# Performance work log

Hardware: AMD Instinct MI355X
Metric: run time of the kernel (lower is better)

The kernel has to match this reference:

```python
import jax, jax.numpy as jnp
import numpy as np

V = 17  # number of skeleton joints (hard-coded in the torch module)
NUM_SUBSET = 3

def _dam_mask():
    # Reproduces the Python masking loops: zero block [12:17,12:17] and rows/cols {3,6,7,9,10}
    m = np.ones((V, V), np.float32)
    m[12:17, 12:17] = 0.0
    for j in (3, 6, 7, 9, 10):
        m[j, :] = 0.0
        m[:, j] = 0.0
    return jnp.asarray(m)

def setup_inputs() -> dict:
    key = jax.random.key(0)
    ks = jax.random.split(key, 8)
    N, Cin, Cout, T, G = 64, 64, 64, 256, 8
    return {
        "x": jax.random.normal(ks[0], (N, Cin, T, V), jnp.float32),
        "A_base": jax.random.uniform(ks[1], (NUM_SUBSET, V, V), jnp.float32),  # fixed adjacency buffer
        "DA": 0.01 * jax.random.normal(ks[2], (NUM_SUBSET, G, V, V), jnp.float32),   # DecoupleA param
        "DAM": 0.01 * jax.random.normal(ks[3], (NUM_SUBSET, G, V, V), jnp.float32),  # DecoupleAM param (masked, detached)
        "conv_w": jax.random.normal(ks[4], (NUM_SUBSET * Cout, Cin), jnp.float32) * (2.0 / Cin) ** 0.5,  # 1x1 conv
        "conv_b": jnp.zeros((NUM_SUBSET * Cout,), jnp.float32),
        "se_w": jax.random.normal(ks[5], (3,), jnp.float32) * 0.5,  # conv2_1: Conv1d(1,1,k=3,pad=1,no bias)
        "bn_gamma": jnp.full((Cout,), 1e-6, jnp.float32),  # bn_init(bn, 1e-6)
        "bn_beta": jnp.zeros((Cout,), jnp.float32),
    }

def reference(x, A_base, DA, DAM, conv_w, conv_b, se_w, bn_gamma, bn_beta):
    G = DA.shape[1]
    Cout = bn_gamma.shape[0]
    N, Cin, T, _ = x.shape
    # --- adjacency assembly: A (buffer, broadcast over groups) + DecoupleA + masked DecoupleAM ---
    A = A_base[:, None] + DA + DAM * _dam_mask()              # [3, G, V, V]
    # torch .repeat(1, out//groups, 1, 1) tiles along channel axis; + 0.04 from A_final loop
    A_final = jnp.tile(A, (1, Cout // G, 1, 1)) + 0.04        # [3, Cout, V, V]
    # --- 1x1 conv C_in -> 3*C_out ---
    m = jnp.einsum('nctv,kc->nktv', x, conv_w) + conv_b[None, :, None, None]
    m = m.reshape(N, NUM_SUBSET, Cout, T, V)
    # --- grouped adjacency aggregation (A_final has no batch dependence) ---
    m = jnp.einsum('nkctv,kcvw->nctw', m, A_final)            # [N, Cout, T, V]
    # --- SE-style channel attention: global avg pool -> Conv1d(k=3) over channels -> sigmoid gate ---
    p = m.mean(axis=(2, 3))                                   # [N, Cout]
    pp = jnp.pad(p, ((0, 0), (1, 1)))
    g = se_w[0] * pp[:, :-2] + se_w[1] * pp[:, 1:-1] + se_w[2] * pp[:, 2:]
    q = m + m * jax.nn.sigmoid(g)[:, :, None, None]
    # --- BatchNorm2d (training mode: batch stats over N,T,V) ---
    mu = q.mean(axis=(0, 2, 3), keepdims=True)
    var = q.var(axis=(0, 2, 3), keepdims=True)
    q = bn_gamma[None, :, None, None] * (q - mu) * jax.lax.rsqrt(var + 1e-5) + bn_beta[None, :, None, None]
    # --- residual (down == identity since in_channels == out_channels) and ReLU ---
    return jax.nn.relu(q + x)
```

## Files before the change

### kernel.cpp

```cpp
#include <hip/hip_runtime.h>
#include <math.h>

#define NN 64
#define CIN 64
#define COUT 64
#define TT 256
#define VV 17
#define NSUB 3
#define GG 8

#define WS_MB 0
#define WS_WBF 12288
#define WS_PSUM 18432
#define WS_SSQ 22528
#define WS_ACOEF 0
#define WS_BCOEF 4096
#define M2BF_BYTE_OFF 131072ull
#define M2BF_NEED (M2BF_BYTE_OFF + 2ull * 64 * 64 * 256 * 17)

typedef short bh8 __attribute__((ext_vector_type(8)));
typedef float f32x4 __attribute__((ext_vector_type(4)));
typedef float f32x16 __attribute__((ext_vector_type(16)));
typedef unsigned short u16t;

__device__ __forceinline__ unsigned bf16r(float f) {
    unsigned u = __builtin_bit_cast(unsigned, f);
    return (u + 0x7fffu + ((u >> 16) & 1u)) >> 16;
}
__device__ __forceinline__ float bf2f(unsigned us) {
    return __builtin_bit_cast(float, us << 16);
}

__device__ __forceinline__ float mfull(const float* Ab, const float* DA, const float* DAM,
                                       int s, int g, int v, int w) {
    const unsigned bad = (1u << 3) | (1u << 6) | (1u << 7) | (1u << 9) | (1u << 10);
    float mask = ((v >= 12 && w >= 12) || ((bad >> v) & 1) || ((bad >> w) & 1)) ? 0.f : 1.f;
    int src = ((s * GG + g) * VV + v) * VV + w;
    return Ab[(s * VV + v) * VV + w] + DA[src] + DAM[src] * mask + 0.04f;
}

__global__ void gcn_prep(const float* __restrict__ Ab, const float* __restrict__ DA,
                         const float* __restrict__ DAM, const float* __restrict__ convw,
                         float* __restrict__ ws) {
    int t0 = blockIdx.x * 256 + threadIdx.x;
    int stride = gridDim.x * 256;
    u16t* wbf = (u16t*)(ws + WS_WBF);
    for (int i = t0; i < 192 * 64; i += stride) wbf[i] = (u16t)bf16r(convw[i]);
    u16t* mb = (u16t*)(ws + WS_MB);
    for (int i = t0; i < NSUB * GG * 32 * 32; i += stride) {
        int k = i & 31, w = (i >> 5) & 31, g = (i >> 10) & 7, s = i >> 13;
        u16t val = 0;
        if (w < VV && k < VV) val = (u16t)bf16r(mfull(Ab, DA, DAM, s, g, k, w));
        mb[i] = val;
    }
    for (int i = t0; i < 8192; i += stride) ws[WS_PSUM + i] = 0.f;
}

template <int BFOUT>
__global__ __launch_bounds__(512, 4) void gcn_pass1(const float* __restrict__ x,
                                                    const float* __restrict__ convb,
                                                    const float* __restrict__ ws,
                                                    float* __restrict__ out,
                                                    u16t* __restrict__ m2b,
                                                    float* __restrict__ psum,
                                                    float* __restrict__ ssq) {
    __shared__ __align__(16) unsigned char smem[73984];
    u16t* xsT = (u16t*)smem;
    u16t* Wl = (u16t*)(smem + 20736);
    u16t* mt = (u16t*)(smem + 48384);

    const int tid = threadIdx.x;
    const int wv = tid >> 6;
    const int l = tid & 63;
    const int c16 = l & 15;
    const int q4 = (l >> 4) & 3;
    const int c32 = l & 31;
    const int hi = l >> 5;
    const int n = blockIdx.x >> 3;

    {
        const unsigned* wsrc = (const unsigned*)(ws + WS_WBF);
        unsigned* wd = (unsigned*)Wl;
        for (int j = tid; j < 192 * 32; j += 512) wd[(j >> 5) * 36 + (j & 31)] = wsrc[j];
        unsigned* mz = (unsigned*)mt;
        for (int j = tid; j < 6400; j += 512) mz[j] = 0u;
    }

    const u16t* mb16 = (const u16t*)(ws + WS_MB);
    bh8 Badj[3], Badj2[3];
#pragma unroll
    for (int s = 0; s < 3; ++s) {
        const u16t* mrow = &mb16[((s * 8 + wv) * 32 + c32) * 32 + 8 * hi];
        Badj[s] = *(const bh8*)mrow;
        Badj2[s] = *(const bh8*)(mrow + 16);
    }

    float acc1[8], acc2[8];
#pragma unroll
    for (int j = 0; j < 8; ++j) { acc1[j] = 0.f; acc2[j] = 0.f; }

    for (int k4 = 0; k4 < 4; ++k4) {
        const int tt = (blockIdx.x & 7) * 4 + k4;

        const float* xb = x + (size_t)n * 64 * 4352 + tt * 136;
        for (int task = tid; task < 136 * 8; task += 512) {
            int oct = task / 136;
            int col = task - 136 * oct;
            const float* src = xb + (8 * oct) * 4352 + col;
            float r0 = src[0], r1 = src[4352], r2 = src[2 * 4352], r3 = src[3 * 4352];
            float r4 = src[4 * 4352], r5 = src[5 * 4352], r6 = src[6 * 4352], r7 = src[7 * 4352];
            uint4 pk;
            pk.x = bf16r(r0) | (bf16r(r1) << 16);
            pk.y = bf16r(r2) | (bf16r(r3) << 16);
            pk.z = bf16r(r4) | (bf16r(r5) << 16);
            pk.w = bf16r(r6) | (bf16r(r7) << 16);
            *(uint4*)&((unsigned*)xsT)[col * 36 + oct * 4] = pk;
        }
        __syncthreads();

        bh8 Bc[2], Bc8[2];
#pragma unroll
        for (int ks = 0; ks < 2; ++ks)
            Bc[ks] = *(const bh8*)&xsT[(16 * wv + c16) * 72 + 32 * ks + 8 * q4];
        if (wv < 4) {
#pragma unroll
            for (int ks = 0; ks < 2; ++ks)
                Bc8[ks] = *(const bh8*)&xsT[(128 + c16) * 72 + 32 * ks + 8 * q4];
        }

        f32x16 D2[2];
        D2[0] = 0; D2[1] = 0;

#pragma unroll
        for (int s = 0; s < 3; ++s) {
            f32x4 Dc[4], Dc8;
#pragma unroll
            for (int rf = 0; rf < 4; ++rf)
                Dc[rf] = *(const f32x4*)(convb + s * 64 + 16 * rf + 4 * q4);
            if (wv < 4) Dc8 = *(const f32x4*)(convb + s * 64 + 16 * wv + 4 * q4);
#pragma unroll
            for (int ks = 0; ks < 2; ++ks)
#pragma unroll
                for (int rf = 0; rf < 4; ++rf) {
                    bh8 A = *(const bh8*)&Wl[(s * 64 + 16 * rf + c16) * 72 + 32 * ks + 8 * q4];
                    Dc[rf] = __builtin_amdgcn_mfma_f32_16x16x32_bf16(A, Bc[ks], Dc[rf], 0, 0, 0);
                }
            if (wv < 4) {
#pragma unroll
                for (int ks = 0; ks < 2; ++ks) {
                    bh8 A = *(const bh8*)&Wl[(s * 64 + 16 * wv + c16) * 72 + 32 * ks + 8 * q4];
                    Dc8 = __builtin_amdgcn_mfma_f32_16x16x32_bf16(A, Bc8[ks], Dc8, 0, 0, 0);
                }
            }

            if (s > 0) __syncthreads();
            {
                int col = 16 * wv + c16;
                int t = (col * 241) >> 12;
                int v = col - 17 * t;
                int off = t * 24 + v;
#pragma unroll
                for (int rf = 0; rf < 4; ++rf) {
                    int co0 = 16 * rf + 4 * q4;
#pragma unroll
                    for (int i = 0; i < 4; ++i)
                        mt[(co0 + i) * 200 + off] = (u16t)bf16r(Dc[rf][i]);
                }
                if (wv < 4 && c16 < 8) {
                    int v8 = (128 + c16) - 119;
                    int off8 = 7 * 24 + v8;
                    int co0 = 16 * wv + 4 * q4;
#pragma unroll
                    for (int i = 0; i < 4; ++i)
                        mt[(co0 + i) * 200 + off8] = (u16t)bf16r(Dc8[i]);
                }
            }
            __syncthreads();

#pragma unroll
            for (int p = 0; p < 2; ++p) {
                int co = wv + 8 * ((c32 >> 3) + 4 * p);
                int base = co * 200 + (c32 & 7) * 24 + 8 * hi;
                bh8 a0 = *(const bh8*)&mt[base];
                bh8 a1 = *(const bh8*)&mt[base + 16];
                D2[p] = __builtin_amdgcn_mfma_f32_32x32x16_bf16(a0, Badj[s], D2[p], 0, 0, 0);
                D2[p] = __builtin_amdgcn_mfma_f32_32x32x16_bf16(a1, Badj2[s], D2[p], 0, 0, 0);
            }
        }

        u16t* stg = xsT;
#pragma unroll
        for (int p = 0; p < 2; ++p)
#pragma unroll
            for (int reg = 0; reg < 16; ++reg) {
                int row = (reg & 3) + 8 * (reg >> 2) + 4 * hi;
                int cosel = row >> 3;
                int t = row & 7;
                int co = wv + 8 * (cosel + 4 * p);
                float val = D2[p][reg];
                if (c32 < 17) stg[co * 140 + t * 17 + c32] = (u16t)bf16r(val);
                int j = cosel + 4 * p;
                acc1[j] += val;
                acc2[j] += val * val;
            }
        __syncthreads();

        if (BFOUT) {
            u16t* gm = m2b + (size_t)n * 64 * 4352 + tt * 136;
#pragma unroll
            for (int it = 0; it < 5; ++it) {
                int c = tid + 512 * it;
                if (c < 2176) {
                    int co = c / 34;
                    int pos = c - 34 * co;
                    *(uint2*)(gm + co * 4352 + pos * 4) = *(const uint2*)&stg[co * 140 + pos * 4];
                }
            }
        } else {
            float* ob = out + (size_t)n * 64 * 4352 + tt * 136;
#pragma unroll
            for (int it = 0; it < 5; ++it) {
                int c = tid + 512 * it;
                if (c < 2176) {
                    int co = c / 34;
                    int pos = c - 34 * co;
                    uint2 u = *(const uint2*)&stg[co * 140 + pos * 4];
                    float4 v;
                    v.x = bf2f(u.x & 0xffffu);
                    v.y = bf2f(u.x >> 16);
                    v.z = bf2f(u.y & 0xffffu);
                    v.w = bf2f(u.y >> 16);
                    *(float4*)(ob + co * 4352 + pos * 4) = v;
                }
            }
        }
        __syncthreads();
    }

#pragma unroll
    for (int j = 0; j < 8; ++j) {
        float s1 = acc1[j], s2 = acc2[j];
#pragma unroll
        for (int m = 1; m < 64; m <<= 1) {
            s1 += __shfl_xor(s1, m);
            s2 += __shfl_xor(s2, m);
        }
        if (l == 0) {
            atomicAdd(&psum[n * 64 + wv + 8 * j], s1);
            atomicAdd(&ssq[n * 64 + wv + 8 * j], s2);
        }
    }
}

__global__ void gcn_stats(const float* __restrict__ se_w, const float* __restrict__ gamma,
                          const float* __restrict__ beta, float* __restrict__ ws) {
    __shared__ float ps[4096], sc[4096], q2s[4096];
    __shared__ float mu_s[64], inv_s[64];
    int tid = threadIdx.x;
    const float* psum = ws + WS_PSUM;
    const float* ssq = ws + WS_SSQ;
    float* acoef = ws + WS_ACOEF;
    float* bcoef = ws + WS_BCOEF;
    for (int i = tid; i < 4096; i += 256) ps[i] = psum[i] * (1.f / (TT * VV));
    __syncthreads();
    float w0 = se_w[0], w1 = se_w[1], w2 = se_w[2];
    for (int i = tid; i < 4096; i += 256) {
        int c = i & 63;
        float pm = (c > 0) ? ps[i - 1] : 0.f;
        float pp = (c < 63) ? ps[i + 1] : 0.f;
        float gg = w0 * pm + w1 * ps[i] + w2 * pp;
        float s = 1.f + 1.f / (1.f + expf(-gg));
        sc[i] = s;
        q2s[i] = s * s * ssq[i];
    }
    __syncthreads();
    if (tid < 64) {
        float mu = 0.f, e2 = 0.f;
        for (int nn = 0; nn < 64; ++nn) {
            mu += sc[nn * 64 + tid] * ps[nn * 64 + tid];
            e2 += q2s[nn * 64 + tid];
        }
        mu *= (1.f / 64.f);
        e2 *= (1.f / (64.f * TT * VV));
        float var = e2 - mu * mu;
        mu_s[tid] = mu;
        inv_s[tid] = rsqrtf(var + 1e-5f);
    }
    __syncthreads();
    for (int i = tid; i < 4096; i += 256) {
        int c = i & 63;
        float gin = gamma[c] * inv_s[c];
        acoef[i] = gin * sc[i];
        bcoef[i] = beta[c] - gin * mu_s[c];
    }
}

__global__ __launch_bounds__(256) void gcn_final_f32(const float* __restrict__ x,
                                                     const float* __restrict__ ws,
                                                     float* __restrict__ out) {
    const float* acoef = ws + WS_ACOEF;
    const float* bcoef = ws + WS_BCOEF;
    int i = blockIdx.x * 256 + threadIdx.x;
    const int total4 = (NN * COUT * TT * VV) / 4;
    if (i >= total4) return;
    int nc = i / ((TT * VV) / 4);
    float a = acoef[nc], b = bcoef[nc];
    float4 m = ((const float4*)out)[i];
    float4 xx = ((const float4*)x)[i];
    float4 r;
    r.x = fmaxf(fmaf(a, m.x, b) + xx.x, 0.f);
    r.y = fmaxf(fmaf(a, m.y, b) + xx.y, 0.f);
    r.z = fmaxf(fmaf(a, m.z, b) + xx.z, 0.f);
    r.w = fmaxf(fmaf(a, m.w, b) + xx.w, 0.f);
    ((float4*)out)[i] = r;
}

__global__ __launch_bounds__(256) void gcn_final_bf16(const float* __restrict__ x,
                                                      const float* __restrict__ ws,
                                                      const u16t* __restrict__ m2b,
                                                      float* __restrict__ out) {
    const float* acoef = ws + WS_ACOEF;
    const float* bcoef = ws + WS_BCOEF;
    int i = blockIdx.x * 256 + threadIdx.x;
    const int total8 = (NN * COUT * TT * VV) / 8;
    if (i >= total8) return;
    int nc = i / 544;
    float a = acoef[nc], b = bcoef[nc];
    uint4 u = *(const uint4*)(m2b + 8 * (size_t)i);
    float4 x0 = ((const float4*)x)[2 * i];
    float4 x1 = ((const float4*)x)[2 * i + 1];
    float4 r0, r1;
    r0.x = fmaxf(fmaf(a, bf2f(u.x & 0xffffu), b) + x0.x, 0.f);
    r0.y = fmaxf(fmaf(a, bf2f(u.x >> 16), b) + x0.y, 0.f);
    r0.z = fmaxf(fmaf(a, bf2f(u.y & 0xffffu), b) + x0.z, 0.f);
    r0.w = fmaxf(fmaf(a, bf2f(u.y >> 16), b) + x0.w, 0.f);
    r1.x = fmaxf(fmaf(a, bf2f(u.z & 0xffffu), b) + x1.x, 0.f);
    r1.y = fmaxf(fmaf(a, bf2f(u.z >> 16), b) + x1.y, 0.f);
    r1.z = fmaxf(fmaf(a, bf2f(u.w & 0xffffu), b) + x1.z, 0.f);
    r1.w = fmaxf(fmaf(a, bf2f(u.w >> 16), b) + x1.w, 0.f);
    ((float4*)out)[2 * i] = r0;
    ((float4*)out)[2 * i + 1] = r1;
}

extern "C" void kernel_launch(void* const* d_in, const int* in_sizes, int n_in,
                              void* d_out, int out_size, void* d_ws, size_t ws_size,
                              hipStream_t stream) {
    const float* x = (const float*)d_in[0];
    const float* Ab = (const float*)d_in[1];
    const float* DA = (const float*)d_in[2];
    const float* DAM = (const float*)d_in[3];
    const float* convw = (const float*)d_in[4];
    const float* convb = (const float*)d_in[5];
    const float* sew = (const float*)d_in[6];
    const float* gamma = (const float*)d_in[7];
    const float* beta = (const float*)d_in[8];
    float* out = (float*)d_out;
    float* ws = (float*)d_ws;
    u16t* m2b = (u16t*)((char*)d_ws + M2BF_BYTE_OFF);
    const bool bfpath = ws_size >= M2BF_NEED;

    gcn_prep<<<16, 256, 0, stream>>>(Ab, DA, DAM, convw, ws);
    if (bfpath) {
        gcn_pass1<1><<<512, 512, 0, stream>>>(x, convb, ws, out, m2b,
                                              ws + WS_PSUM, ws + WS_SSQ);
        gcn_stats<<<1, 256, 0, stream>>>(sew, gamma, beta, ws);
        const int total8 = (NN * COUT * TT * VV) / 8;
        gcn_final_bf16<<<(total8 + 255) / 256, 256, 0, stream>>>(x, ws, m2b, out);
    } else {
        gcn_pass1<0><<<512, 512, 0, stream>>>(x, convb, ws, out, m2b,
                                              ws + WS_PSUM, ws + WS_SSQ);
        gcn_stats<<<1, 256, 0, stream>>>(sew, gamma, beta, ws);
        const int total4 = (NN * COUT * TT * VV) / 4;
        gcn_final_f32<<<(total4 + 255) / 256, 256, 0, stream>>>(x, ws, out);
    }
}
```

Before: 131.5 us.

## Prefetch next x tile into registers and store bf16 intermediate tile-contiguous

The x tile for the next time-chunk is loaded into registers during the current chunk's MFMA work, so global load latency overlaps with compute instead of stalling before the barrier. The bf16 intermediate is now written as contiguous per-(n,tt) blocks of 8704 elements using 16-byte stores instead of strided 8-byte stores. The final kernel is restructured to read these blocks, one block per (n,tt). This adds register pressure from the 16-float prefetch buffer, and the staging pitch changes to 144.

```diff
diff --git a/kernel.cpp b/kernel.cpp
--- a/kernel.cpp
+++ b/kernel.cpp
@@ -99,22 +99,43 @@
 #pragma unroll
     for (int j = 0; j < 8; ++j) { acc1[j] = 0.f; acc2[j] = 0.f; }
 
+    const int oct0 = tid / 136, col0 = tid - 136 * oct0;
+    const int t1i = tid + 512;
+    const int oct1 = t1i / 136, col1 = t1i - 136 * oct1;
+
+    float xr[16];
+    {
+        const float* xb = x + (size_t)n * 278528 + ((blockIdx.x & 7) * 4) * 136;
+        const float* s0 = xb + (8 * oct0) * 4352 + col0;
+        const float* s1 = xb + (8 * oct1) * 4352 + col1;
+#pragma unroll
+        for (int k = 0; k < 8; ++k) { xr[k] = s0[k * 4352]; xr[8 + k] = s1[k * 4352]; }
+    }
+
     for (int k4 = 0; k4 < 4; ++k4) {
         const int tt = (blockIdx.x & 7) * 4 + k4;
 
-        const float* xb = x + (size_t)n * 64 * 4352 + tt * 136;
-        for (int task = tid; task < 136 * 8; task += 512) {
-            int oct = task / 136;
-            int col = task - 136 * oct;
-            const float* src = xb + (8 * oct) * 4352 + col;
-            float r0 = src[0], r1 = src[4352], r2 = src[2 * 4352], r3 = src[3 * 4352];
-            float r4 = src[4 * 4352], r5 = src[5 * 4352], r6 = src[6 * 4352], r7 = src[7 * 4352];
+        {
             uint4 pk;
-            pk.x = bf16r(r0) | (bf16r(r1) << 16);
-            pk.y = bf16r(r2) | (bf16r(r3) << 16);
-            pk.z = bf16r(r4) | (bf16r(r5) << 16);
-            pk.w = bf16r(r6) | (bf16r(r7) << 16);
-            *(uint4*)&((unsigned*)xsT)[col * 36 + oct * 4] = pk;
+            pk.x = bf16r(xr[0]) | (bf16r(xr[1]) << 16);
+            pk.y = bf16r(xr[2]) | (bf16r(xr[3]) << 16);
+            pk.z = bf16r(xr[4]) | (bf16r(xr[5]) << 16);
+            pk.w = bf16r(xr[6]) | (bf16r(xr[7]) << 16);
+            *(uint4*)&((unsigned*)xsT)[col0 * 36 + oct0 * 4] = pk;
+            pk.x = bf16r(xr[8]) | (bf16r(xr[9]) << 16);
+            pk.y = bf16r(xr[10]) | (bf16r(xr[11]) << 16);
+            pk.z = bf16r(xr[12]) | (bf16r(xr[13]) << 16);
+            pk.w = bf16r(xr[14]) | (bf16r(xr[15]) << 16);
+            *(uint4*)&((unsigned*)xsT)[col1 * 36 + oct1 * 4] = pk;
+        }
+        if (tid < 64) {
+            const float* src = x + (size_t)n * 278528 + tt * 136 + 56 * 4352 + (72 + tid);
+            uint4 pk;
+            pk.x = bf16r(src[0]) | (bf16r(src[4352]) << 16);
+            pk.y = bf16r(src[2 * 4352]) | (bf16r(src[3 * 4352]) << 16);
+            pk.z = bf16r(src[4 * 4352]) | (bf16r(src[5 * 4352]) << 16);
+            pk.w = bf16r(src[6 * 4352]) | (bf16r(src[7 * 4352]) << 16);
+            *(uint4*)&((unsigned*)xsT)[(72 + tid) * 36 + 28] = pk;
         }
         __syncthreads();
 
@@ -126,6 +147,14 @@
 #pragma unroll
             for (int ks = 0; ks < 2; ++ks)
                 Bc8[ks] = *(const bh8*)&xsT[(128 + c16) * 72 + 32 * ks + 8 * q4];
+        }
+
+        if (k4 < 3) {
+            const float* xb = x + (size_t)n * 278528 + (tt + 1) * 136;
+            const float* s0 = xb + (8 * oct0) * 4352 + col0;
+            const float* s1 = xb + (8 * oct1) * 4352 + col1;
+#pragma unroll
+            for (int k = 0; k < 8; ++k) { xr[k] = s0[k * 4352]; xr[8 + k] = s1[k * 4352]; }
         }
 
         f32x16 D2[2];
@@ -198,7 +227,7 @@
                 int t = row & 7;
                 int co = wv + 8 * (cosel + 4 * p);
                 float val = D2[p][reg];
-                if (c32 < 17) stg[co * 140 + t * 17 + c32] = (u16t)bf16r(val);
+                if (c32 < 17) stg[co * 144 + t * 17 + c32] = (u16t)bf16r(val);
                 int j = cosel + 4 * p;
                 acc1[j] += val;
                 acc2[j] += val * val;
@@ -206,25 +235,24 @@
         __syncthreads();
 
         if (BFOUT) {
-            u16t* gm = m2b + (size_t)n * 64 * 4352 + tt * 136;
+            u16t* gm = m2b + (size_t)(n * 32 + tt) * 8704;
+#pragma unroll
+            for (int it = 0; it < 3; ++it) {
+                int c = tid + 512 * it;
+                if (c < 1088) {
+                    int co = c / 17, j = c - 17 * co;
+                    *(uint4*)(gm + 8 * c) = *(const uint4*)&stg[co * 144 + 8 * j];
+                }
+            }
+        } else {
+            float* ob = out + (size_t)n * 64 * 4352 + tt * 136;
 #pragma unroll
             for (int it = 0; it < 5; ++it) {
                 int c = tid + 512 * it;
                 if (c < 2176) {
                     int co = c / 34;
                     int pos = c - 34 * co;
-                    *(uint2*)(gm + co * 4352 + pos * 4) = *(const uint2*)&stg[co * 140 + pos * 4];
-                }
-            }
-        } else {
-            float* ob = out + (size_t)n * 64 * 4352 + tt * 136;
-#pragma unroll
-            for (int it = 0; it < 5; ++it) {
-                int c = tid + 512 * it;
-                if (c < 2176) {
-                    int co = c / 34;
-                    int pos = c - 34 * co;
-                    uint2 u = *(const uint2*)&stg[co * 140 + pos * 4];
+                    uint2 u = *(const uint2*)&stg[co * 144 + pos * 4];
                     float4 v;
                     v.x = bf2f(u.x & 0xffffu);
                     v.y = bf2f(u.x >> 16);
@@ -321,25 +349,35 @@
                                                       float* __restrict__ out) {
     const float* acoef = ws + WS_ACOEF;
     const float* bcoef = ws + WS_BCOEF;
-    int i = blockIdx.x * 256 + threadIdx.x;
-    const int total8 = (NN * COUT * TT * VV) / 8;
-    if (i >= total8) return;
-    int nc = i / 544;
-    float a = acoef[nc], b = bcoef[nc];
-    uint4 u = *(const uint4*)(m2b + 8 * (size_t)i);
-    float4 x0 = ((const float4*)x)[2 * i];
-    float4 x1 = ((const float4*)x)[2 * i + 1];
-    float4 r0, r1;
-    r0.x = fmaxf(fmaf(a, bf2f(u.x & 0xffffu), b) + x0.x, 0.f);
-    r0.y = fmaxf(fmaf(a, bf2f(u.x >> 16), b) + x0.y, 0.f);
-    r0.z = fmaxf(fmaf(a, bf2f(u.y & 0xffffu), b) + x0.z, 0.f);
-    r0.w = fmaxf(fmaf(a, bf2f(u.y >> 16), b) + x0.w, 0.f);
-    r1.x = fmaxf(fmaf(a, bf2f(u.z & 0xffffu), b) + x1.x, 0.f);
-    r1.y = fmaxf(fmaf(a, bf2f(u.z >> 16), b) + x1.y, 0.f);
-    r1.z = fmaxf(fmaf(a, bf2f(u.w & 0xffffu), b) + x1.z, 0.f);
-    r1.w = fmaxf(fmaf(a, bf2f(u.w >> 16), b) + x1.w, 0.f);
-    ((float4*)out)[2 * i] = r0;
-    ((float4*)out)[2 * i + 1] = r1;
+    const int bt = blockIdx.x;
+    const int n = bt >> 5, tt = bt & 31;
+    const u16t* gm = m2b + (size_t)bt * 8704;
+    const size_t base = (size_t)n * 278528 + tt * 136;
+    const int tid = threadIdx.x;
+#pragma unroll
+    for (int it = 0; it < 5; ++it) {
+        int task = tid + 256 * it;
+        if (task < 1088) {
+            int co = task / 17, j = task - 17 * co;
+            float a = acoef[n * 64 + co], b = bcoef[n * 64 + co];
+            uint4 u = *(const uint4*)(gm + 8 * task);
+            const float* xp = x + base + co * 4352 + 8 * j;
+            float4 x0 = *(const float4*)xp;
+            float4 x1 = *(const float4*)(xp + 4);
+            float4 r0, r1;
+            r0.x = fmaxf(fmaf(a, bf2f(u.x & 0xffffu), b) + x0.x, 0.f);
+            r0.y = fmaxf(fmaf(a, bf2f(u.x >> 16), b) + x0.y, 0.f);
+            r0.z = fmaxf(fmaf(a, bf2f(u.y & 0xffffu), b) + x0.z, 0.f);
+            r0.w = fmaxf(fmaf(a, bf2f(u.y >> 16), b) + x0.w, 0.f);
+            r1.x = fmaxf(fmaf(a, bf2f(u.z & 0xffffu), b) + x1.x, 0.f);
+            r1.y = fmaxf(fmaf(a, bf2f(u.z >> 16), b) + x1.y, 0.f);
+            r1.z = fmaxf(fmaf(a, bf2f(u.w & 0xffffu), b) + x1.z, 0.f);
+            r1.w = fmaxf(fmaf(a, bf2f(u.w >> 16), b) + x1.w, 0.f);
+            float* op = out + base + co * 4352 + 8 * j;
+            *(float4*)op = r0;
+            *(float4*)(op + 4) = r1;
+        }
+    }
 }
 
 extern "C" void kernel_launch(void* const* d_in, const int* in_sizes, int n_in,
@@ -364,8 +402,7 @@
         gcn_pass1<1><<<512, 512, 0, stream>>>(x, convb, ws, out, m2b,
                                               ws + WS_PSUM, ws + WS_SSQ);
         gcn_stats<<<1, 256, 0, stream>>>(sew, gamma, beta, ws);
-        const int total8 = (NN * COUT * TT * VV) / 8;
-        gcn_final_bf16<<<(total8 + 255) / 256, 256, 0, stream>>>(x, ws, m2b, out);
+        gcn_final_bf16<<<2048, 256, 0, stream>>>(x, ws, m2b, out);
     } else {
         gcn_pass1<0><<<512, 512, 0, stream>>>(x, convb, ws, out, m2b,
                                               ws + WS_PSUM, ws + WS_SSQ);
```

Result: slower. 142.4 us (+8.3%).
